# Kernel optimization log

Measured on AMD Instinct MI355X. Metric: run time of the kernel, lower is better.

Reference implementation:

```python
import jax, jax.numpy as jnp
from jax import lax
import numpy as np


def make_hippo_matrix(N):
    P = np.sqrt(1 + 2 * np.arange(N))
    A = P[:, None] * P[None, :]
    A = np.tril(A) - np.diag(np.arange(N))
    return jnp.asarray(-A, dtype=jnp.float32)


def setup_inputs() -> dict:
    key = jax.random.key(0)
    k1, k2, k3, k4, k5 = jax.random.split(key, 5)
    Bsz, L, H, N = 16, 2048, 512, 64
    dt_min, dt_max = 0.001, 0.1
    u = jax.random.normal(k1, (Bsz, L, H), dtype=jnp.float32)
    B_ssm = jax.random.normal(k2, (N, 1), dtype=jnp.float32)
    C_ssm = jax.random.normal(k3, (1, N), dtype=jnp.float32)
    D_skip = jax.random.normal(k4, (1,), dtype=jnp.float32)
    log_dt = (jax.random.uniform(k5, (1,), dtype=jnp.float32)
              * (np.log(dt_max) - np.log(dt_min)) + np.log(dt_min))
    return {"u": u, "B_ssm": B_ssm, "C_ssm": C_ssm, "D_skip": D_skip, "log_dt": log_dt}


def reference(u, B_ssm, C_ssm, D_skip, log_dt):
    Bsz, L, H = u.shape
    N = B_ssm.shape[0]
    A = make_hippo_matrix(N)  # fixed HiPPO buffer (non-trainable)

    # --- discretize: A_bar = expm(dt*A); B_bar = A^{-1} (A_bar - I) B ---
    dt = jnp.exp(log_dt)  # (1,)
    A_bar = jax.scipy.linalg.expm(dt * A)  # (N, N)
    B_bar = jnp.linalg.solve(A, (A_bar - jnp.eye(N, dtype=A.dtype)) @ B_ssm)  # (N, 1)

    # --- kernel K[k] = C @ A_bar^k @ B_bar, k = 0..L-1, via scan ---
    def step(power, _):
        kk = (C_ssm @ power)[0, 0]
        return A_bar @ power, kk
    _, K = lax.scan(step, B_bar, None, length=L)  # (L,)

    # torch F.conv1d is cross-correlation; with padding L-1 and keeping the
    # first L outputs this equals a causal convolution with the FLIPPED kernel:
    #   y[t] = sum_{m=0}^{t} K[L-1-m] * u[t-m]
    Krev = K[::-1]
    n_fft = 2 * L  # linear (non-circular) convolution
    Uf = jnp.fft.rfft(u, n=n_fft, axis=1)            # (B, n_fft//2+1, H)
    Kf = jnp.fft.rfft(Krev, n=n_fft)                 # (n_fft//2+1,)
    y_conv = jnp.fft.irfft(Uf * Kf[None, :, None], n=n_fft, axis=1)[:, :L, :]
    y = y_conv.astype(u.dtype) + D_skip * u
    return y
```

## Files before the change

kernel.cpp:

```cpp
#include <hip/hip_runtime.h>
#include <math.h>


typedef short short8 __attribute__((ext_vector_type(8)));
typedef short short4v __attribute__((ext_vector_type(4)));
typedef float f32x4 __attribute__((ext_vector_type(4)));

#define SWMASK 28
__device__ __forceinline__ int swz(int r, int c) {
  return (r << 6) + (c ^ (r & SWMASK));
}
__device__ __forceinline__ unsigned rne_bf16(float x) {
  unsigned u = __float_as_uint(x);
  return (u + 0x7FFFu + ((u >> 16) & 1u)) >> 16;
}
__device__ __forceinline__ float invfact(int k) {
  switch (k) {
    case 0: return 1.0f;            case 1: return 1.0f;
    case 2: return 0.5f;            case 3: return (float)(1.0/6.0);
    case 4: return (float)(1.0/24.0);       case 5: return (float)(1.0/120.0);
    case 6: return (float)(1.0/720.0);      case 7: return (float)(1.0/5040.0);
    case 8: return (float)(1.0/40320.0);    default: return (float)(1.0/362880.0);
  }
}
__device__ __forceinline__ int slotU(int row, int kg) {
  return (row << 6) + ((kg ^ (row & 7)) << 3);
}
__device__ __forceinline__ float bf2f(unsigned short s) {
  return __uint_as_float(((unsigned)s) << 16);
}
__device__ __forceinline__ unsigned short bfh(float x) {
  return (unsigned short)rne_bf16(x);
}
__device__ __forceinline__ unsigned short bfl(float x, unsigned short h) {
  return (unsigned short)rne_bf16(x - __uint_as_float(((unsigned)h) << 16));
}

__device__ __forceinline__ void mmMFMA(
    const unsigned short* rowLh, const unsigned short* rowLl,
    const unsigned short* colRh, const unsigned short* colRl,
    unsigned short* oColH, unsigned short* oColL,
    unsigned short* oRowH, unsigned short* oRowL,
    float* oF32, const float* Xg, float cI, float cX, int tid) {
  const int lane = tid & 63, w = tid >> 6;
  const int wr = w & 3, wc = w >> 2;
  const int g = lane >> 4, m = lane & 15;
  const bool doN = (oColH != nullptr) || (oF32 != nullptr);
  const bool doT = (oRowH != nullptr);
  f32x4 an = (f32x4){0.f, 0.f, 0.f, 0.f};
  f32x4 at = (f32x4){0.f, 0.f, 0.f, 0.f};

  if (doN) {
#pragma unroll
    for (int kt = 0; kt < 2; ++kt) {
      short8 ah = *(const short8*)&rowLh[slotU(16 * wr + m, 4 * kt + g)];
      short8 al = *(const short8*)&rowLl[slotU(16 * wr + m, 4 * kt + g)];
      short8 bh = *(const short8*)&colRh[slotU(16 * wc + m, 4 * kt + g)];
      short8 bl = *(const short8*)&colRl[slotU(16 * wc + m, 4 * kt + g)];
      an = __builtin_amdgcn_mfma_f32_16x16x32_bf16(ah, bh, an, 0, 0, 0);
      an = __builtin_amdgcn_mfma_f32_16x16x32_bf16(ah, bl, an, 0, 0, 0);
      an = __builtin_amdgcn_mfma_f32_16x16x32_bf16(al, bh, an, 0, 0, 0);
    }
    if (Xg) {
#pragma unroll
      for (int r = 0; r < 4; ++r) {
        int rc = 16 * wr + 4 * g + r, cc = 16 * wc + m;
        float gv = cX * Xg[(rc << 6) + (cc ^ (rc & 28))];
        if (rc == cc) gv += cI;
        an[r] += gv;
      }
    }
  }
  if (doT) {
#pragma unroll
    for (int kt = 0; kt < 2; ++kt) {
      short8 ah = *(const short8*)&colRh[slotU(16 * wr + m, 4 * kt + g)];
      short8 al = *(const short8*)&colRl[slotU(16 * wr + m, 4 * kt + g)];
      short8 bh = *(const short8*)&rowLh[slotU(16 * wc + m, 4 * kt + g)];
      short8 bl = *(const short8*)&rowLl[slotU(16 * wc + m, 4 * kt + g)];
      at = __builtin_amdgcn_mfma_f32_16x16x32_bf16(ah, bh, at, 0, 0, 0);
      at = __builtin_amdgcn_mfma_f32_16x16x32_bf16(ah, bl, at, 0, 0, 0);
      at = __builtin_amdgcn_mfma_f32_16x16x32_bf16(al, bh, at, 0, 0, 0);
    }
    if (Xg) {
      int rc = 16 * wc + m;
      int cb = 16 * wr + 4 * g;
      f32x4 xv = *(const f32x4*)&Xg[(rc << 6) + (cb ^ (rc & 28))];
#pragma unroll
      for (int r = 0; r < 4; ++r) {
        float gv = cX * xv[r];
        if (rc == cb + r) gv += cI;
        at[r] += gv;
      }
    }
  }
  __syncthreads();
  const int k0 = 16 * wr + 4 * g;
  if (doN) {
    if (oColH) {
      short4v h4, l4;
#pragma unroll
      for (int r = 0; r < 4; ++r) {
        unsigned short h = bfh(an[r]);
        h4[r] = (short)h;
        l4[r] = (short)bfl(an[r], h);
      }
      int s = slotU(16 * wc + m, k0 >> 3) + (k0 & 7);
      *(short4v*)&oColH[s] = h4;
      *(short4v*)&oColL[s] = l4;
    }
    if (oF32) {
#pragma unroll
      for (int r = 0; r < 4; ++r) {
        int rc = k0 + r;
        oF32[(rc << 6) + ((16 * wc + m) ^ (rc & 28))] = an[r];
      }
    }
  }
  if (doT) {
    short4v h4, l4;
#pragma unroll
    for (int r = 0; r < 4; ++r) {
      unsigned short h = bfh(at[r]);
      h4[r] = (short)h;
      l4[r] = (short)bfl(at[r], h);
    }
    int s = slotU(16 * wc + m, k0 >> 3) + (k0 & 7);
    *(short4v*)&oRowH[s] = h4;
    *(short4v*)&oRowL[s] = l4;
  }
  __syncthreads();
}

__global__ __launch_bounds__(1024, 1) void prep_quant(
    const float* __restrict__ u, const float* __restrict__ B_ssm,
    const float* __restrict__ C_ssm, const float* __restrict__ D_skip,
    const float* __restrict__ log_dt, uint4* __restrict__ rg_hi,
    uint4* __restrict__ rg_lo, int* __restrict__ wsi,
    uint4* __restrict__ ubf) {
  __shared__ __align__(16) float smem[16384];
  const int tid = threadIdx.x;

  if (blockIdx.x != 0) {
    int q = blockIdx.x - 1;
    int b = q >> 7, rem = q & 127;
    int tc = rem >> 1, hf = rem & 1;
    int t0 = (tc << 5) + (hf << 4);
    float* S = smem;
#pragma unroll
    for (int r = 0; r < 2; ++r) {
      int s = tid + (r << 10);
      int row = s >> 7, c4 = (s & 127) << 2;
      float4 v = *(const float4*)(u + ((((b << 11) + t0 + row) << 9) + c4));
      *(float4*)&S[row * 520 + c4] = v;
    }
    __syncthreads();
    {
      int gidx = tid;
      int jnG = gidx >> 5;
      int gl = (gidx >> 4) & 1;
      int hm = gidx & 15;
      int gg = (hf << 1) | gl;
      int h = (jnG << 4) + hm;
      int tb = gl << 3;
      unsigned pk[4];
#pragma unroll
      for (int q2 = 0; q2 < 4; ++q2) {
        unsigned lo = rne_bf16(S[(tb + 2 * q2) * 520 + h]);
        unsigned hi = rne_bf16(S[(tb + 2 * q2 + 1) * 520 + h]);
        pk[q2] = lo | (hi << 16);
      }
      ubf[(((b << 6) | tc) << 11) | (jnG << 6) | (gg << 4) | hm] =
          make_uint4(pk[0], pk[1], pk[2], pk[3]);
    }
    return;
  }

  float* b0 = smem;
  float* b1 = smem + 4096;
  float* b2 = smem + 8192;
  float* b3 = smem + 12288;
  unsigned short* RH = (unsigned short*)b2;
  unsigned short* RL = RH + 4096;
  unsigned short* CH = (unsigned short*)b3;
  unsigned short* CL = CH + 4096;
  unsigned short* X2H = (unsigned short*)b1;
  unsigned short* X2L = X2H + 4096;
  double* Pd = (double*)b3;
  const int lane = tid & 63, wv = tid >> 6;
  const float dtf = expf(log_dt[0]);

  if (tid < 64) {
    double p = sqrt(2.0 * tid + 1.0);
    Pd[tid] = p;
    double s = p;
#pragma unroll
    for (int off = 1; off < 64; off <<= 1) {
      double t = __shfl_down(s, off, 64);
      if (tid + off < 64) s += t;
    }
    b2[tid] = (float)((tid + 1.0) + p * (s - p));
  }
  __syncthreads();
  float maxc = 0.f;
  for (int j = 0; j < 64; ++j) maxc = fmaxf(maxc, b2[j]);
  int iE;
  frexpf(dtf * maxc, &iE);
  int sExp = iE > 0 ? iE : 0;
  const float scale = ldexpf(dtf, -sExp);
  __syncthreads();

  const int r0i = (tid & 15) << 2, c0i = ((tid >> 4) & 15) << 2;
  double pr_[4], pc_[4];
  float xv[4][4];
  if (tid < 256) {
#pragma unroll
    for (int i = 0; i < 4; ++i) pr_[i] = Pd[r0i + i];
#pragma unroll
    for (int j = 0; j < 4; ++j) pc_[j] = Pd[c0i + j];
  }
  __syncthreads();
  if (tid < 256) {
    unsigned short xh[4][4], xl[4][4];
#pragma unroll
    for (int i = 0; i < 4; ++i)
#pragma unroll
      for (int j = 0; j < 4; ++j) {
        int ri = r0i + i, cj = c0i + j;
        float a;
        if (ri > cj)       a = -(float)(pr_[i] * pc_[j]);
        else if (ri == cj) a = -(float)(ri + 1);
        else               a = 0.0f;
        float x = scale * a;
        xv[i][j] = x;
        xh[i][j] = bfh(x);
        xl[i][j] = bfl(x, xh[i][j]);
        b0[swz(ri, cj)] = x;
      }
#pragma unroll
    for (int i = 0; i < 4; ++i) {
      short4v h4, l4;
#pragma unroll
      for (int j = 0; j < 4; ++j) { h4[j] = (short)xh[i][j]; l4[j] = (short)xl[i][j]; }
      int s = slotU(r0i + i, c0i >> 3) + (c0i & 7);
      *(short4v*)&RH[s] = h4;
      *(short4v*)&RL[s] = l4;
    }
#pragma unroll
    for (int j = 0; j < 4; ++j) {
      short4v h4, l4;
#pragma unroll
      for (int i = 0; i < 4; ++i) { h4[i] = (short)xh[i][j]; l4[i] = (short)xl[i][j]; }
      int s = slotU(c0i + j, r0i >> 3) + (r0i & 7);
      *(short4v*)&CH[s] = h4;
      *(short4v*)&CL[s] = l4;
    }
  }
  __syncthreads();

  mmMFMA(RH, RL, CH, CL, X2H, X2L, nullptr, nullptr, nullptr, nullptr,
         0.f, 0.f, tid);

  if (tid < 256) {
#pragma unroll
    for (int i = 0; i < 4; ++i) {
      short4v h4, l4;
#pragma unroll
      for (int j = 0; j < 4; ++j) {
        float gv = invfact(9) * xv[i][j];
        if (r0i + i == c0i + j) gv += invfact(8);
        unsigned short h = bfh(gv);
        h4[j] = (short)h;
        l4[j] = (short)bfl(gv, h);
      }
      int s = slotU(r0i + i, c0i >> 3) + (c0i & 7);
      *(short4v*)&RH[s] = h4;
      *(short4v*)&RL[s] = l4;
    }
  }
  __syncthreads();

  for (int mq = 3; mq >= 1; --mq)
    mmMFMA(RH, RL, X2H, X2L, nullptr, nullptr, RH, RL, nullptr, b0,
           invfact(2 * mq), invfact(2 * mq + 1), tid);
  mmMFMA(RH, RL, X2H, X2L, CH, CL, RH, RL, b1, b0, 0.f, 1.f, tid);

  for (int q = 0; q < sExp; ++q)
    mmMFMA(RH, RL, CH, CL, CH, CL, RH, RL, b1, b1, 0.f, 2.f, tid);

  float* Bl = b0 + 64;
  if (tid < 64) {
    Bl[tid] = B_ssm[tid];
    int d = tid;
    float x = b1[(d << 6) + (d ^ (d & 28))] + 1.0f;
    unsigned short h = bfh(x), l = bfl(x, h);
    int s = slotU(d, d >> 3) + (d & 7);
    RH[s] = h; RL[s] = l; CH[s] = h; CL[s] = l;
  }
  __syncthreads();

  if (tid < 64) {
    int i = tid;
    double pi = sqrt(2.0 * i + 1.0);
    double accd = 0.0;
#pragma unroll
    for (int k4 = 0; k4 < 16; ++k4) {
      int jM = (k4 << 2) ^ (i & 28);
      float4 mv = *(const float4*)&b1[(i << 6) + jM];
      float4 bv = *(const float4*)&Bl[k4 << 2];
      accd += (double)mv.x * bv.x + (double)mv.y * bv.y +
              (double)mv.z * bv.z + (double)mv.w * bv.w;
    }
    double xvv = 0.0;
    for (int j = 0; j < 64; ++j) {
      if (i == j) xvv = accd / (-(double)(j + 1));
      double xj = __shfl(xvv, j, 64);
      double pj = __shfl(pi, j, 64);
      if (i > j) accd += pi * pj * xj;
    }
    b0[i] = (float)xvv;
    b1[(i << 6) + (i ^ (i & 28))] += 1.0f;
  }
  __syncthreads();

  for (int k = 0; k < 6; ++k) {
    int cnt = 1 << k;
    for (int t = wv; t < cnt; t += 16) {
      float a0 = 0.f, a1 = 0.f;
#pragma unroll
      for (int k4 = 0; k4 < 16; ++k4) {
        int jM = (k4 << 2) ^ (lane & 28);
        f32x4 mv = *(const f32x4*)&b1[(lane << 6) + jM];
        f32x4 vvv = *(const f32x4*)&b0[(t << 6) + ((k4 << 2) ^ (t & 28))];
        a0 = fmaf(mv[0], vvv[0], fmaf(mv[1], vvv[1], a0));
        a1 = fmaf(mv[2], vvv[2], fmaf(mv[3], vvv[3], a1));
      }
      int td = t + cnt;
      b0[(td << 6) + (lane ^ (td & 28))] = a0 + a1;
    }
    mmMFMA(RH, RL, CH, CL, CH, CL, RH, RL, b1, nullptr, 0.f, 0.f, tid);
  }

  if (tid < 64) b1[tid] = C_ssm[tid];
  __syncthreads();
  for (int k = 0; k < 5; ++k) {
    int cnt = 1 << k;
    for (int t = wv; t < cnt; t += 16) {
      float ah = 0.f, al = 0.f;
#pragma unroll
      for (int kg = 0; kg < 8; ++kg) {
        short8 ch8 = *(const short8*)&CH[slotU(lane, kg)];
        short8 cl8 = *(const short8*)&CL[slotU(lane, kg)];
        f32x4 w0 = *(const f32x4*)&b1[(t << 6) + (kg << 3)];
        f32x4 w1 = *(const f32x4*)&b1[(t << 6) + (kg << 3) + 4];
#pragma unroll
        for (int j = 0; j < 4; ++j) {
          ah = fmaf(bf2f((unsigned short)ch8[j]), w0[j], ah);
          al = fmaf(bf2f((unsigned short)cl8[j]), w0[j], al);
        }
#pragma unroll
        for (int j = 0; j < 4; ++j) {
          ah = fmaf(bf2f((unsigned short)ch8[4 + j]), w1[j], ah);
          al = fmaf(bf2f((unsigned short)cl8[4 + j]), w1[j], al);
        }
      }
      b1[((t + cnt) << 6) + lane] = ah + al;
    }
    if (k < 3) {
      mmMFMA(RH, RL, CH, CL, CH, CL, RH, RL, nullptr, nullptr, 0.f, 0.f, tid);
    } else if (k == 3) {
      mmMFMA(RH, RL, CH, CL, CH, CL, nullptr, nullptr, nullptr, nullptr,
             0.f, 0.f, tid);
    } else {
      __syncthreads();
    }
  }

  float* K = b3;
  for (int x = tid; x < 2048; x += 1024) {
    int tp = x >> 6, t = x & 63;
    float d0 = 0.f, d1 = 0.f;
#pragma unroll
    for (int i4 = 0; i4 < 64; i4 += 4) {
      f32x4 wv4 = *(const f32x4*)&b1[(tp << 6) + i4];
      f32x4 vv4 = *(const f32x4*)&b0[(t << 6) + (i4 ^ (t & 28))];
      d0 = fmaf(wv4[0], vv4[0], fmaf(wv4[1], vv4[1], d0));
      d1 = fmaf(wv4[2], vv4[2], fmaf(wv4[3], vv4[3], d1));
    }
    K[x] = d0 + d1;
  }
  __syncthreads();

  unsigned short* kh = (unsigned short*)b2;
  unsigned short* kl = kh + 2192;
  float* ss = (float*)(kh + 4400);
  const float D = D_skip[0];
  for (int x = tid; x < 2192; x += 1024) {
    float v = 0.f;
    if (x < 2048) { v = K[x]; if (x == 2047) v += D; }
    unsigned h = rne_bf16(v);
    float hf2 = __uint_as_float(h << 16);
    unsigned l = rne_bf16(v - hf2);
    kh[x] = (unsigned short)h;
    kl[x] = (unsigned short)l;
  }
  if (tid < 256) {
    float ssum = 0.f;
#pragma unroll
    for (int q = 0; q < 8; ++q) {
      int x = (tid << 3) + q;
      float v = K[x];
      if (x == 2047) v += D;
      ssum += v * v;
    }
    ss[tid] = ssum;
  }
  __syncthreads();

  for (int e = tid; e < 2176; e += 1024) {
    unsigned ph[4], pl[4];
#pragma unroll
    for (int q2 = 0; q2 < 4; ++q2) {
      ph[q2] = (unsigned)kh[e + 2 * q2] | ((unsigned)kh[e + 2 * q2 + 1] << 16);
      pl[q2] = (unsigned)kl[e + 2 * q2] | ((unsigned)kl[e + 2 * q2 + 1] << 16);
    }
    rg_hi[e] = make_uint4(ph[0], ph[1], ph[2], ph[3]);
    rg_lo[e] = make_uint4(pl[0], pl[1], pl[2], pl[3]);
  }
  if (tid == 0) {
    float accq = 0.f;
    int xt = 0;
    for (int jc = 255; jc >= 0; --jc) {
      float na = accq + ss[jc];
      if (na > 4e-8f) { xt = (jc + 1) << 3; break; }
      accq = na;
    }
    wsi[0] = 2048 - xt;
  }
}

__device__ __forceinline__ void load_bfrag(short8* bf, const uint4* ubf,
                                           const float* u, int use_ubf, int b,
                                           int kt, int h0, int wn, int lane) {
  if (use_ubf) {
    const short8* base = (const short8*)(ubf + ((((b << 6) | kt) << 11) |
                                               (((h0 >> 4) + (wn << 2)) << 6) |
                                               lane));
#pragma unroll
    for (int j = 0; j < 4; ++j) bf[j] = base[j << 6];
  } else {
    int gg = lane >> 4, hm = lane & 15;
#pragma unroll
    for (int j = 0; j < 4; ++j) {
      const float* src = u + ((((b << 11) + (kt << 5) + (gg << 3)) << 9) + h0 +
                              (((wn << 2) + j) << 4) + hm);
      unsigned pk[4];
#pragma unroll
      for (int q = 0; q < 4; ++q) {
        unsigned lo = rne_bf16(src[q << 10]);
        unsigned hi = rne_bf16(src[(q << 10) + 512]);
        pk[q] = lo | (hi << 16);
      }
      uint4 vv = make_uint4(pk[0], pk[1], pk[2], pk[3]);
      bf[j] = __builtin_bit_cast(short8, vv);
    }
  }
}

__global__ __launch_bounds__(256) void conv_kernel(
    const float* __restrict__ u, const uint4* __restrict__ rg_hi,
    const uint4* __restrict__ rg_lo, const uint4* __restrict__ ubf,
    const int* __restrict__ wsi, float* __restrict__ y, int use_ubf) {
  __shared__ __align__(16) unsigned ringh[1024], ringl[1024];
  const int tid = threadIdx.x;
  const int bid0 = blockIdx.x;
  const int bid = ((bid0 & 7) << 6) | (bid0 >> 3);
  const int b = bid >> 5;
  const int bn = bid & 3;
  const int pr = (bid >> 2) & 7;
  const int h0 = bn << 7;
  const int lane = tid & 63, w = tid >> 6;
  const int wm = w & 1, wn = w >> 1;
  const int g = lane >> 4, m = lane & 15;
  const int D_lo = wsi[0];

  for (int tile = 0; tile < 2; ++tile) {
    const int bm = tile ? pr : 15 - pr;
    const int l0 = bm << 7;
    const int e0 = 1920 - l0;
    const int ktiles = 4 * bm + 4;
    int kt_lim = ((l0 + 127 - D_lo) >> 5) + 1;
    if (kt_lim < 0) kt_lim = 0;
    if (kt_lim > ktiles) kt_lim = ktiles;

    __syncthreads();
    for (int tsk = tid; tsk < 432; tsk += 256) {
      int isLo = tsk >= 216;
      int e = e0 + (isLo ? tsk - 216 : tsk);
      if (e <= 2175) {
        uint4 v = isLo ? rg_lo[e] : rg_hi[e];
        ((uint4*)(isLo ? ringl : ringh))[e & 255] = v;
      }
    }

    f32x4 acc[4][4];
#pragma unroll
    for (int i = 0; i < 4; ++i)
#pragma unroll
      for (int j = 0; j < 4; ++j) acc[i][j] = (f32x4){0.f, 0.f, 0.f, 0.f};

    short8 bcur[4];
    if (kt_lim > 0) load_bfrag(bcur, ubf, u, use_ubf, b, 0, h0, wn, lane);

    for (int kt = 0; kt < kt_lim; ++kt) {
      __syncthreads();
      uint4 tv;
      bool tdo = false;
      int tslot = 0;
      const bool tlo = (tid >= 32);
      if (tid < 64) {
        int te = e0 + 216 + (kt << 5) + (tid & 31);
        if (te <= 2175) {
          tv = tlo ? rg_lo[te] : rg_hi[te];
          tdo = true;
          tslot = te & 255;
        }
      }
      const int ebase = 2047 - l0 + (kt << 5) - (wm << 6) - m + (g << 3);
      short8 ah[4], al[4];
#pragma unroll
      for (int i = 0; i < 4; ++i) {
        int slot = (ebase - (i << 4)) & 255;
        ah[i] = ((const short8*)ringh)[slot];
        al[i] = ((const short8*)ringl)[slot];
      }
      short8 bnx[4];
      if (kt + 1 < kt_lim)
        load_bfrag(bnx, ubf, u, use_ubf, b, kt + 1, h0, wn, lane);
#pragma unroll
      for (int i = 0; i < 4; ++i)
#pragma unroll
        for (int j = 0; j < 4; ++j) {
          acc[i][j] = __builtin_amdgcn_mfma_f32_16x16x32_bf16(ah[i], bcur[j],
                                                              acc[i][j], 0, 0, 0);
          acc[i][j] = __builtin_amdgcn_mfma_f32_16x16x32_bf16(al[i], bcur[j],
                                                              acc[i][j], 0, 0, 0);
        }
      if (tdo) ((uint4*)(tlo ? ringl : ringh))[tslot] = tv;
      if (kt + 1 < kt_lim) {
#pragma unroll
        for (int j = 0; j < 4; ++j) bcur[j] = bnx[j];
      }
    }

#pragma unroll
    for (int i = 0; i < 4; ++i)
#pragma unroll
      for (int j = 0; j < 4; ++j) {
        int l = l0 + (wm << 6) + (i << 4) + (g << 2);
        int h = h0 + (((wn << 2) + j) << 4) + m;
        int off = (((b << 11) + l) << 9) + h;
#pragma unroll
        for (int r = 0; r < 4; ++r) y[off + (r << 9)] = acc[i][j][r];
      }
  }
}

extern "C" void kernel_launch(void* const* d_in, const int* in_sizes, int n_in,
                              void* d_out, int out_size, void* d_ws,
                              size_t ws_size, hipStream_t stream) {
  (void)in_sizes; (void)n_in; (void)out_size;
  const float* u = (const float*)d_in[0];
  const float* B_ssm = (const float*)d_in[1];
  const float* C_ssm = (const float*)d_in[2];
  const float* D_skip = (const float*)d_in[3];
  const float* log_dt = (const float*)d_in[4];
  float* y = (float*)d_out;

  const size_t UBF_BYTES = (size_t)16 * 64 * 2048 * 16;
  const size_t RG_BYTES = (size_t)2176 * 16 * 2 + 256;
  int use_ubf = (ws_size >= UBF_BYTES + RG_BYTES) ? 1 : 0;
  char* wsb = (char*)d_ws;
  uint4* ubf = (uint4*)wsb;
  uint4* rg_hi = use_ubf ? (uint4*)(wsb + UBF_BYTES) : (uint4*)wsb;
  uint4* rg_lo = rg_hi + 2176;
  int* wsi = (int*)(rg_lo + 2176);

  prep_quant<<<use_ubf ? 2049 : 1, 1024, 0, stream>>>(
      u, B_ssm, C_ssm, D_skip, log_dt, rg_hi, rg_lo, wsi, ubf);
  conv_kernel<<<512, 256, 0, stream>>>(u, rg_hi, rg_lo, ubf, wsi, y, use_ubf);
}
```

Measured before the change: 202.5 us.

## Process two k-tiles per barrier with swizzled LDS ring and deeper B prefetch

Unrolls the conv main loop to handle two 32-wide k-tiles per __syncthreads, refilling 64 ring entries per iteration instead of 32 and shrinking the initial ring preload. It also applies an XOR swizzle to the LDS ring slot to reduce bank conflicts, and prefetches B fragments two tiles ahead. Launch bounds now request two blocks per SM. The goal is to halve barrier count and hide global latency, at the cost of more registers held across the loop.

```diff
diff --git a/kernel.cpp b/kernel.cpp
--- a/kernel.cpp
+++ b/kernel.cpp
@@ -34,6 +34,10 @@
 }
 __device__ __forceinline__ unsigned short bfl(float x, unsigned short h) {
   return (unsigned short)rne_bf16(x - __uint_as_float(((unsigned)h) << 16));
+}
+__device__ __forceinline__ int rslot(int e) {
+  int s = e & 255;
+  return s ^ ((s >> 3) & 7);
 }
 
 __device__ __forceinline__ void mmMFMA(
@@ -467,7 +471,7 @@
   }
 }
 
-__global__ __launch_bounds__(256) void conv_kernel(
+__global__ __launch_bounds__(256, 2) void conv_kernel(
     const float* __restrict__ u, const uint4* __restrict__ rg_hi,
     const uint4* __restrict__ rg_lo, const uint4* __restrict__ ubf,
     const int* __restrict__ wsi, float* __restrict__ y, int use_ubf) {
@@ -494,12 +498,12 @@
     if (kt_lim > ktiles) kt_lim = ktiles;
 
     __syncthreads();
-    for (int tsk = tid; tsk < 432; tsk += 256) {
-      int isLo = tsk >= 216;
-      int e = e0 + (isLo ? tsk - 216 : tsk);
+    for (int tsk = tid; tsk < 368; tsk += 256) {
+      int isLo = tsk >= 184;
+      int e = e0 + (isLo ? tsk - 184 : tsk);
       if (e <= 2175) {
         uint4 v = isLo ? rg_lo[e] : rg_hi[e];
-        ((uint4*)(isLo ? ringl : ringh))[e & 255] = v;
+        ((uint4*)(isLo ? ringl : ringh))[rslot(e)] = v;
       }
     }
 
@@ -509,47 +513,75 @@
 #pragma unroll
       for (int j = 0; j < 4; ++j) acc[i][j] = (f32x4){0.f, 0.f, 0.f, 0.f};
 
-    short8 bcur[4];
+    short8 bcur[4], bnext[4];
     if (kt_lim > 0) load_bfrag(bcur, ubf, u, use_ubf, b, 0, h0, wn, lane);
-
-    for (int kt = 0; kt < kt_lim; ++kt) {
+    if (kt_lim > 1) load_bfrag(bnext, ubf, u, use_ubf, b, 1, h0, wn, lane);
+
+    for (int ks = 0; ks < kt_lim; ks += 2) {
       __syncthreads();
       uint4 tv;
       bool tdo = false;
       int tslot = 0;
-      const bool tlo = (tid >= 32);
-      if (tid < 64) {
-        int te = e0 + 216 + (kt << 5) + (tid & 31);
+      const bool tlo = (tid >= 64);
+      if (tid < 128) {
+        int te = e0 + 184 + (ks << 5) + (tid & 63);
         if (te <= 2175) {
           tv = tlo ? rg_lo[te] : rg_hi[te];
           tdo = true;
-          tslot = te & 255;
+          tslot = rslot(te);
         }
       }
-      const int ebase = 2047 - l0 + (kt << 5) - (wm << 6) - m + (g << 3);
-      short8 ah[4], al[4];
-#pragma unroll
-      for (int i = 0; i < 4; ++i) {
-        int slot = (ebase - (i << 4)) & 255;
-        ah[i] = ((const short8*)ringh)[slot];
-        al[i] = ((const short8*)ringl)[slot];
-      }
-      short8 bnx[4];
-      if (kt + 1 < kt_lim)
-        load_bfrag(bnx, ubf, u, use_ubf, b, kt + 1, h0, wn, lane);
-#pragma unroll
-      for (int i = 0; i < 4; ++i)
-#pragma unroll
-        for (int j = 0; j < 4; ++j) {
-          acc[i][j] = __builtin_amdgcn_mfma_f32_16x16x32_bf16(ah[i], bcur[j],
-                                                              acc[i][j], 0, 0, 0);
-          acc[i][j] = __builtin_amdgcn_mfma_f32_16x16x32_bf16(al[i], bcur[j],
-                                                              acc[i][j], 0, 0, 0);
+      short8 bA[4], bB[4];
+      {
+        const int ebase = 2047 - l0 + (ks << 5) - (wm << 6) - m + (g << 3);
+        short8 ah[4], al[4];
+#pragma unroll
+        for (int i = 0; i < 4; ++i) {
+          int s = rslot(ebase - (i << 4));
+          ah[i] = ((const short8*)ringh)[s];
+          al[i] = ((const short8*)ringl)[s];
         }
+        if (ks + 2 < kt_lim)
+          load_bfrag(bA, ubf, u, use_ubf, b, ks + 2, h0, wn, lane);
+#pragma unroll
+        for (int i = 0; i < 4; ++i)
+#pragma unroll
+          for (int j = 0; j < 4; ++j) {
+            acc[i][j] = __builtin_amdgcn_mfma_f32_16x16x32_bf16(
+                ah[i], bcur[j], acc[i][j], 0, 0, 0);
+            acc[i][j] = __builtin_amdgcn_mfma_f32_16x16x32_bf16(
+                al[i], bcur[j], acc[i][j], 0, 0, 0);
+          }
+      }
+      if (ks + 1 < kt_lim) {
+        const int ebase = 2047 - l0 + ((ks + 1) << 5) - (wm << 6) - m + (g << 3);
+        short8 ah[4], al[4];
+#pragma unroll
+        for (int i = 0; i < 4; ++i) {
+          int s = rslot(ebase - (i << 4));
+          ah[i] = ((const short8*)ringh)[s];
+          al[i] = ((const short8*)ringl)[s];
+        }
+        if (ks + 3 < kt_lim)
+          load_bfrag(bB, ubf, u, use_ubf, b, ks + 3, h0, wn, lane);
+#pragma unroll
+        for (int i = 0; i < 4; ++i)
+#pragma unroll
+          for (int j = 0; j < 4; ++j) {
+            acc[i][j] = __builtin_amdgcn_mfma_f32_16x16x32_bf16(
+                ah[i], bnext[j], acc[i][j], 0, 0, 0);
+            acc[i][j] = __builtin_amdgcn_mfma_f32_16x16x32_bf16(
+                al[i], bnext[j], acc[i][j], 0, 0, 0);
+          }
+      }
       if (tdo) ((uint4*)(tlo ? ringl : ringh))[tslot] = tv;
-      if (kt + 1 < kt_lim) {
-#pragma unroll
-        for (int j = 0; j < 4; ++j) bcur[j] = bnx[j];
+      if (ks + 2 < kt_lim) {
+#pragma unroll
+        for (int j = 0; j < 4; ++j) bcur[j] = bA[j];
+      }
+      if (ks + 3 < kt_lim) {
+#pragma unroll
+        for (int j = 0; j < 4; ++j) bnext[j] = bB[j];
       }
     }
 
```

Result: no change. 204.5 us (+1.0%).
